# Optimization experiments

Hardware: AMD Instinct MI355X
Metric: run time of the kernel (lower is better)

Reference implementation:

```python
import jax, jax.numpy as jnp
import numpy as np

TAU = 2.0     # membrane decay constant (init arg tau)
ALPHA = 1.0   # surrogate-gradient width (self.alpha() == 1.0)

# PiecewiseQuadratic surrogate spike: heaviside fwd, quadratic-band bwd
@jax.custom_vjp
def spike(v):
    return (v >= 0.0).astype(v.dtype)

def _spike_fwd(v):
    return spike(v), v

def _spike_bwd(v, g):
    sg = jnp.where(jnp.abs(v) > 1.0 / ALPHA, 0.0, -ALPHA * ALPHA * jnp.abs(v) + ALPHA)
    return (g * sg.astype(g.dtype),)

spike.defvjp(_spike_fwd, _spike_bwd)


def setup_inputs() -> dict:
    key = jax.random.key(0)
    x = jax.random.normal(key, (64, 64, 8192), dtype=jnp.float32)  # [B, T, F]
    return {
        "x": x,
        "momentum": jnp.array([0.9], dtype=jnp.float32),
        "lamb": jnp.array([0.5], dtype=jnp.float32),
        "thresholds": jnp.array([1.0], dtype=jnp.float32),
    }


def reference(x, momentum, lamb, thresholds):
    # regular=False -> lamb used directly (no sigmoid)
    mt = momentum[0]
    lb = lamb[0]
    th = thresholds[0]
    xt = jnp.moveaxis(x, 1, 0)  # [T, B, F] for scan over time
    u0 = jnp.zeros_like(xt[0])
    m0 = jnp.zeros_like(xt[0])

    def step(carry, xi):
        u_last, m = carry
        u = u_last / TAU + xi
        s = spike(u - th)
        m = mt * m + (1.0 - mt) * (u - u_last)
        u_next = (u * lb + m * (1.0 - lb)) * (1.0 - s)
        return (u_next, m), s

    _, out = jax.lax.scan(step, (u0, m0), xt)
    return jnp.moveaxis(out, 0, 1)  # [B, T, F]
```

## Files before the change

kernel.cpp:

```cpp
#include <hip/hip_runtime.h>


constexpr int B = 64;
constexpr int T = 64;
constexpr int F = 8192;
constexpr int S   = 4;
constexpr int DLT = 16;

template <int GLO, int GHI>
__device__ __forceinline__ void run_phase(
    int tau0, const int* base, float* u, float* m,
    const float* __restrict__ x, float* __restrict__ out,
    float mt, float omt, float lb, float olb, float th)
{
#pragma clang fp contract(off)
#pragma unroll
    for (int k = 0; k < DLT; ++k) {
        const int tau = tau0 + k;
#pragma unroll
        for (int g = GLO; g <= GHI; ++g) {
            const int t   = tau - DLT * g;
            const int idx = base[g] + t * F;
            const float xv = x[idx];
            const float uu = u[g] * 0.5f + xv;
            const float s  = ((uu - th) >= 0.0f) ? 1.0f : 0.0f;
            const float a  = mt * m[g];
            const float bq = omt * (uu - u[g]);
            m[g] = a + bq;
            u[g] = (uu * lb + m[g] * olb) * (1.0f - s);
            __builtin_nontemporal_store(s, &out[idx]);
        }
    }
}

__global__ __launch_bounds__(256) void lif_fwd_kernel(
    const float* __restrict__ x,
    const float* __restrict__ momentum,
    const float* __restrict__ lamb,
    const float* __restrict__ thresholds,
    float*       __restrict__ out)
{
#pragma clang fp contract(off)
    const int tid = blockIdx.x * blockDim.x + threadIdx.x;
    const int b0  = tid >> 13;
    const int f   = tid & (F - 1);

    const float mt  = momentum[0];
    const float omt = 1.0f - mt;
    const float lb  = lamb[0];
    const float olb = 1.0f - lb;
    const float th  = thresholds[0];

    int   base[S];
    float u[S], m[S];
#pragma unroll
    for (int g = 0; g < S; ++g) {
        base[g] = (b0 + 16 * g) * (T * F) + f;
        u[g] = 0.0f;
        m[g] = 0.0f;
    }

    run_phase<0, 0>(  0, base, u, m, x, out, mt, omt, lb, olb, th);
    run_phase<0, 1>( 16, base, u, m, x, out, mt, omt, lb, olb, th);
    run_phase<0, 2>( 32, base, u, m, x, out, mt, omt, lb, olb, th);
    run_phase<0, 3>( 48, base, u, m, x, out, mt, omt, lb, olb, th);
    run_phase<1, 3>( 64, base, u, m, x, out, mt, omt, lb, olb, th);
    run_phase<2, 3>( 80, base, u, m, x, out, mt, omt, lb, olb, th);
    run_phase<3, 3>( 96, base, u, m, x, out, mt, omt, lb, olb, th);
}

extern "C" void kernel_launch(void* const* d_in, const int* in_sizes, int n_in,
                              void* d_out, int out_size, void* d_ws, size_t ws_size,
                              hipStream_t stream) {
    const float* x   = (const float*)d_in[0];
    const float* mom = (const float*)d_in[1];
    const float* lmb = (const float*)d_in[2];
    const float* thr = (const float*)d_in[3];
    float* out = (float*)d_out;

    const int n_threads = B * F / S;
    const int block = 256;
    const int grid = n_threads / block;
    lif_fwd_kernel<<<grid, block, 0, stream>>>(x, mom, lmb, thr, out);
}
```

Measured before the change: 240.3 us.

## Replace staggered multi-sequence scan with one sequence per thread and register prefetch

```diff
diff --git a/kernel.cpp b/kernel.cpp
--- a/kernel.cpp
+++ b/kernel.cpp
@@ -4,34 +4,7 @@
 constexpr int B = 64;
 constexpr int T = 64;
 constexpr int F = 8192;
-constexpr int S   = 4;
-constexpr int DLT = 16;
-
-template <int GLO, int GHI>
-__device__ __forceinline__ void run_phase(
-    int tau0, const int* base, float* u, float* m,
-    const float* __restrict__ x, float* __restrict__ out,
-    float mt, float omt, float lb, float olb, float th)
-{
-#pragma clang fp contract(off)
-#pragma unroll
-    for (int k = 0; k < DLT; ++k) {
-        const int tau = tau0 + k;
-#pragma unroll
-        for (int g = GLO; g <= GHI; ++g) {
-            const int t   = tau - DLT * g;
-            const int idx = base[g] + t * F;
-            const float xv = x[idx];
-            const float uu = u[g] * 0.5f + xv;
-            const float s  = ((uu - th) >= 0.0f) ? 1.0f : 0.0f;
-            const float a  = mt * m[g];
-            const float bq = omt * (uu - u[g]);
-            m[g] = a + bq;
-            u[g] = (uu * lb + m[g] * olb) * (1.0f - s);
-            __builtin_nontemporal_store(s, &out[idx]);
-        }
-    }
-}
+constexpr int P = 8;
 
 __global__ __launch_bounds__(256) void lif_fwd_kernel(
     const float* __restrict__ x,
@@ -41,8 +14,9 @@
     float*       __restrict__ out)
 {
 #pragma clang fp contract(off)
+
     const int tid = blockIdx.x * blockDim.x + threadIdx.x;
-    const int b0  = tid >> 13;
+    const int b   = tid >> 13;
     const int f   = tid & (F - 1);
 
     const float mt  = momentum[0];
@@ -51,22 +25,36 @@
     const float olb = 1.0f - lb;
     const float th  = thresholds[0];
 
-    int   base[S];
-    float u[S], m[S];
+    const int base = b * (T * F) + f;
+
+    float buf[P];
 #pragma unroll
-    for (int g = 0; g < S; ++g) {
-        base[g] = (b0 + 16 * g) * (T * F) + f;
-        u[g] = 0.0f;
-        m[g] = 0.0f;
+    for (int i = 0; i < P; ++i) buf[i] = x[base + i * F];
+
+    float u = 0.0f, m = 0.0f;
+
+#pragma unroll
+    for (int c = 0; c < T / P; ++c) {
+        float sv[P];
+#pragma unroll
+        for (int j = 0; j < P; ++j) {
+            const int t = c * P + j;
+            const float xv = buf[j];
+            if (t + P < T) buf[j] = x[base + (t + P) * F];
+
+            const float uu = u * 0.5f + xv;
+            const float s  = ((uu - th) >= 0.0f) ? 1.0f : 0.0f;
+            const float a  = mt * m;
+            const float bq = omt * (uu - u);
+            m = a + bq;
+            u = (uu * lb + m * olb) * (1.0f - s);
+            sv[j] = s;
+        }
+#pragma unroll
+        for (int j = 0; j < P; ++j) {
+            __builtin_nontemporal_store(sv[j], &out[base + (c * P + j) * F]);
+        }
     }
-
-    run_phase<0, 0>(  0, base, u, m, x, out, mt, omt, lb, olb, th);
-    run_phase<0, 1>( 16, base, u, m, x, out, mt, omt, lb, olb, th);
-    run_phase<0, 2>( 32, base, u, m, x, out, mt, omt, lb, olb, th);
-    run_phase<0, 3>( 48, base, u, m, x, out, mt, omt, lb, olb, th);
-    run_phase<1, 3>( 64, base, u, m, x, out, mt, omt, lb, olb, th);
-    run_phase<2, 3>( 80, base, u, m, x, out, mt, omt, lb, olb, th);
-    run_phase<3, 3>( 96, base, u, m, x, out, mt, omt, lb, olb, th);
 }
 
 extern "C" void kernel_launch(void* const* d_in, const int* in_sizes, int n_in,
@@ -78,7 +66,7 @@
     const float* thr = (const float*)d_in[3];
     float* out = (float*)d_out;
 
-    const int n_threads = B * F / S;
+    const int n_threads = B * F;
     const int block = 256;
     const int grid = n_threads / block;
     lif_fwd_kernel<<<grid, block, 0, stream>>>(x, mom, lmb, thr, out);
```

Result: no change. 238.2 us (-0.9%).
